# Kernel optimization log

Measured on AMD Instinct MI355X. Metric: run time of the kernel, lower is better.

## Reference

```python
import jax, jax.numpy as jnp
import numpy as np

B, S, HID = 1, 2048, 2048
NH, NKV, HD = 32, 8, 64
ROPE_THETA = 10000.0
NEG = -1e9


def _rope_tables(seq_len, head_dim, theta):
    inv_freq = 1.0 / (theta ** (jnp.arange(0, head_dim, 2, dtype=jnp.float32) / head_dim))
    t = jnp.arange(seq_len, dtype=jnp.float32)
    freqs = jnp.outer(t, inv_freq)            # [S, HD/2]
    emb = jnp.concatenate([freqs, freqs], -1) # [S, HD]
    return jnp.cos(emb), jnp.sin(emb)


def setup_inputs() -> dict:
    key = jax.random.key(0)
    ks = jax.random.split(key, 5)
    sc = 0.02
    hidden_states = jax.random.normal(ks[0], (B, S, HID), jnp.float32)
    Wq = jax.random.normal(ks[1], (NH * HD, HID), jnp.float32) * sc
    Wk = jax.random.normal(ks[2], (NKV * HD, HID), jnp.float32) * sc
    Wv = jax.random.normal(ks[3], (NKV * HD, HID), jnp.float32) * sc
    Wo = jax.random.normal(ks[4], (HID, HID), jnp.float32) * sc
    cos, sin = _rope_tables(S, HD, ROPE_THETA)
    cos = jnp.broadcast_to(cos[None], (B, S, HD))
    sin = jnp.broadcast_to(sin[None], (B, S, HD))
    causal = jnp.tril(jnp.ones((S, S), bool))
    attention_mask = jnp.where(causal, 0.0, NEG).astype(jnp.float32)[None, None]  # [B,1,S,S]
    return {"hidden_states": hidden_states, "Wq": Wq, "Wk": Wk, "Wv": Wv,
            "Wo": Wo, "cos": cos, "sin": sin, "attention_mask": attention_mask}


def _rotate_half(x):
    x1, x2 = jnp.split(x, 2, axis=-1)
    return jnp.concatenate([-x2, x1], axis=-1)


def reference(hidden_states, Wq, Wk, Wv, Wo, cos, sin, attention_mask):
    b, s, _ = hidden_states.shape
    # QKV projections (nn.Linear: x @ W.T), split heads -> [B, H, S, D]
    q = jnp.einsum('bsh,dh->bsd', hidden_states, Wq).reshape(b, s, NH, HD).transpose(0, 2, 1, 3)
    k = jnp.einsum('bsh,dh->bsd', hidden_states, Wk).reshape(b, s, NKV, HD).transpose(0, 2, 1, 3)
    v = jnp.einsum('bsh,dh->bsd', hidden_states, Wv).reshape(b, s, NKV, HD).transpose(0, 2, 1, 3)
    # RoPE (cos/sin broadcast over head dim, unsqueeze_dim=1)
    c = cos[:, None, :, :]
    si = sin[:, None, :, :]
    q = q * c + _rotate_half(q) * si
    k = k * c + _rotate_half(k) * si
    # repeat_kv: GQA groups of 4
    n_rep = NH // NKV
    k = jnp.repeat(k, n_rep, axis=1)
    v = jnp.repeat(v, n_rep, axis=1)
    # Naive materialized attention, softmax in fp32
    scores = jnp.einsum('bhqd,bhkd->bhqk', q, k) / jnp.sqrt(jnp.float32(HD))
    scores = scores + attention_mask
    w = jax.nn.softmax(scores.astype(jnp.float32), axis=-1).astype(q.dtype)
    attn = jnp.einsum('bhqk,bhkd->bhqd', w, v)
    attn = attn.transpose(0, 2, 1, 3).reshape(b, s, NH * HD)
    return jnp.einsum('bsd,od->bso', attn, Wo)
```

## Files before the change

kernel.cpp:

```cpp
#include <hip/hip_runtime.h>
#include <hip/hip_bf16.h>

typedef unsigned short u16;
typedef __bf16 bf16x8 __attribute__((ext_vector_type(8)));
typedef float f32x4 __attribute__((ext_vector_type(4)));

#define S_LEN 2048
#define HID 2048
#define NH 32
#define NKV 8
#define HD 64

__device__ inline u16 f2bf(float x) {
    __bf16 h = (__bf16)x;
    return __builtin_bit_cast(u16, h);
}

__device__ inline void gload_lds16(const u16* g, u16* l) {
    __builtin_amdgcn_global_load_lds((const __attribute__((address_space(1))) unsigned int*)g,
                                     (__attribute__((address_space(3))) unsigned int*)l, 16, 0, 0);
}

__global__ void cvt_all(const float* __restrict__ h, const float* __restrict__ wq,
                        const float* __restrict__ wk, const float* __restrict__ wv,
                        const float* __restrict__ wo,
                        u16* __restrict__ hb, u16* __restrict__ wqkv, u16* __restrict__ wob) {
    int i = blockIdx.x * blockDim.x + threadIdx.x;
    const float* src; u16* dst; int o;
    if (i < 1048576)      { src = h;  dst = hb;   o = i; }
    else if (i < 2097152) { src = wq; dst = wqkv; o = i - 1048576; }
    else if (i < 2359296) { src = wk; dst = wqkv + (size_t)2048 * 2048; o = i - 2097152; }
    else if (i < 2621440) { src = wv; dst = wqkv + (size_t)2560 * 2048; o = i - 2359296; }
    else                  { src = wo; dst = wob;  o = i - 2621440; }
    float4 v = ((const float4*)src)[o];
    ushort4 u;
    u.x = f2bf(v.x); u.y = f2bf(v.y); u.z = f2bf(v.z); u.w = f2bf(v.w);
    ((ushort4*)dst)[o] = u;
}

__global__ __launch_bounds__(256) void gemm_bt(const u16* __restrict__ A,
                                               const u16* __restrict__ B,
                                               void* __restrict__ Cv,
                                               int K_, int mode, int ldc,
                                               const float* __restrict__ cosp,
                                               const float* __restrict__ sinp) {
    __shared__ u16 As[2][64 * 32];
    __shared__ u16 Bs[2][128 * 32];
    const int t = threadIdx.x;
    const int nwg = gridDim.x * gridDim.y;
    const int orig = blockIdx.y * gridDim.x + blockIdx.x;
    const int wgid = (orig & 7) * (nwg >> 3) + (orig >> 3);
    const int bm = wgid % gridDim.x, bn = wgid / gridDim.x;
    const int lane = t & 63, w = t >> 6;
    const int wr2 = (w >> 1) * 32, wc2 = (w & 1) * 64;
    const int g = lane >> 4, r16 = lane & 15;
    f32x4 acc[2][4] = {};

    const int srowA = w * 16 + (lane >> 2);
    const int srowB = w * 32 + (lane >> 2);
    const int scol = (lane & 3) * 8;
    const u16* Ap = A + (size_t)(bm * 64 + srowA) * K_ + scol;
    const u16* Bp = B + (size_t)(bn * 128 + srowB) * K_ + scol;
    const int aoff = w * 512;
    const int boff = w * 1024;

    gload_lds16(Ap, &As[0][aoff]);
    gload_lds16(Bp, &Bs[0][boff]);
    gload_lds16(Bp + (size_t)16 * K_, &Bs[0][boff + 512]);
    __syncthreads();

    int cur = 0;
    for (int kt = 0; kt < K_; kt += 32) {
        const int nxt = kt + 32;
        if (nxt < K_) {
            gload_lds16(Ap + nxt, &As[cur ^ 1][aoff]);
            gload_lds16(Bp + nxt, &Bs[cur ^ 1][boff]);
            gload_lds16(Bp + nxt + (size_t)16 * K_, &Bs[cur ^ 1][boff + 512]);
        }
        bf16x8 af[2], bfr[4];
#pragma unroll
        for (int i = 0; i < 2; i++) af[i] = *(const bf16x8*)(&As[cur][(wr2 + i * 16 + r16) * 32 + g * 8]);
#pragma unroll
        for (int j = 0; j < 4; j++) bfr[j] = *(const bf16x8*)(&Bs[cur][(wc2 + j * 16 + r16) * 32 + g * 8]);
#pragma unroll
        for (int i = 0; i < 2; i++)
#pragma unroll
            for (int j = 0; j < 4; j++)
                acc[i][j] = __builtin_amdgcn_mfma_f32_16x16x32_bf16(af[i], bfr[j], acc[i][j], 0, 0, 0);
        __syncthreads();
        cur ^= 1;
    }

    u16* qb_ = (u16*)Cv;
    u16* kb_ = qb_ + (size_t)2048 * 2048;
    u16* vt_ = kb_ + (size_t)512 * 2048;
    if (mode == 1) {
#pragma unroll
        for (int i = 0; i < 2; i++)
#pragma unroll
            for (int j = 0; j < 4; j++)
#pragma unroll
                for (int r = 0; r < 4; r++) {
                    int row = bm * 64 + wr2 + i * 16 + g * 4 + r;
                    int col = bn * 128 + wc2 + j * 16 + r16;
                    ((float*)Cv)[(size_t)row * ldc + col] = acc[i][j][r];
                }
    } else {
        const int cbase = bn * 128 + wc2;
        if (cbase < 2560) {
            const float scl = (cbase < 2048) ? 0.125f * 1.44269504f : 1.0f;
#pragma unroll
            for (int i = 0; i < 2; i++)
#pragma unroll
                for (int r = 0; r < 4; r++) {
                    int row = bm * 64 + wr2 + i * 16 + g * 4 + r;
#pragma unroll
                    for (int j = 0; j < 2; j++) {
                        int c0 = cbase + j * 16 + r16;
                        int iin = c0 & 63;
                        float x1 = acc[i][j][r], x2 = acc[i][j + 2][r];
                        float cA = cosp[row * 64 + iin],      sA = sinp[row * 64 + iin];
                        float cB = cosp[row * 64 + iin + 32], sB = sinp[row * 64 + iin + 32];
                        u16 o1 = f2bf((x1 * cA - x2 * sA) * scl);
                        u16 o2 = f2bf((x2 * cB + x1 * sB) * scl);
                        if (cbase < 2048) {
                            qb_[(size_t)row * 2048 + c0] = o1;
                            qb_[(size_t)row * 2048 + c0 + 32] = o2;
                        } else {
                            int c = c0 - 2048;
                            int kvh_w = c >> 6, iin2 = c & 63;
                            int gq = (iin2 >> 3) & 3, e = iin2 & 7;
                            int fr = row >> 4, r16w = row & 15;
                            size_t base = ((size_t)(kvh_w * 128 + fr) * 2) * 512 + (size_t)(gq * 16 + r16w) * 8 + e;
                            kb_[base] = o1;
                            kb_[base + 512] = o2;
                        }
                    }
                }
        } else {
#pragma unroll
            for (int i = 0; i < 2; i++)
#pragma unroll
                for (int j = 0; j < 4; j++)
#pragma unroll
                    for (int r = 0; r < 4; r++) {
                        int row = bm * 64 + wr2 + i * 16 + g * 4 + r;
                        int col = cbase + j * 16 + r16;
                        int dg = col - 2560;
                        int kvh_w = dg >> 6, dblk_w = (dg >> 4) & 3, r16v = dg & 15;
                        int fr32 = row >> 5, gv = (row >> 3) & 3, e = row & 7;
                        vt_[((size_t)((kvh_w * 64 + fr32) * 4 + dblk_w)) * 512 + (size_t)(gv * 16 + r16v) * 8 + e] = f2bf(acc[i][j][r]);
                    }
        }
    }
}

__global__ __launch_bounds__(64) void attn_kernel(const u16* __restrict__ q,
                                                  const u16* __restrict__ kp_all,
                                                  const u16* __restrict__ vp_all,
                                                  u16* __restrict__ attn) {
    __shared__ u16 P[2][16][136];
    const int bid = blockIdx.x;
    const int kvh = bid & 7;
    const int h = kvh * 4 + ((bid >> 3) & 3);
    const int p = bid >> 5;
    const int lane = threadIdx.x & 63;
    const int g = lane >> 4, r16 = lane & 15;

    const u16* kp = kp_all + (size_t)kvh * 131072;
    const u16* vp = vp_all + (size_t)kvh * 131072;

    bf16x8 vone;
#pragma unroll
    for (int j = 0; j < 8; j++) vone[j] = (__bf16)1.0f;

    for (int u = 0; u < 2; u++) {
        const int qblk = u ? p : 63 - p;
        const int qrow0 = qblk * 32;

        bf16x8 qf[2][2];
#pragma unroll
        for (int fi = 0; fi < 2; fi++)
#pragma unroll
            for (int d = 0; d < 2; d++)
                qf[fi][d] = *(const bf16x8*)(q + (size_t)(qrow0 + fi * 16 + r16) * (NH * HD) + h * HD + d * 32 + g * 8);

        f32x4 o[2][4] = {};
        f32x4 ol[2] = {};

        const int last = (qrow0 >> 7) << 7;

        bf16x8 kA[4][2], kB[4][2];
#pragma unroll
        for (int s4 = 0; s4 < 4; s4++)
#pragma unroll
            for (int d = 0; d < 2; d++) {
                kA[s4][d] = *(const bf16x8*)(kp + ((size_t)(s4 * 2 + d)) * 512 + lane * 8);
                kB[s4][d] = *(const bf16x8*)(kp + ((size_t)((4 + s4) * 2 + d)) * 512 + lane * 8);
            }

        for (int kv = 0; kv <= last; kv += 128) {
            const bool diag = (kv == last);
            f32x4 sacc[2][8] = {};
#pragma unroll
            for (int s4 = 0; s4 < 4; s4++)
#pragma unroll
                for (int fi = 0; fi < 2; fi++)
#pragma unroll
                    for (int d = 0; d < 2; d++)
                        sacc[fi][s4] = __builtin_amdgcn_mfma_f32_16x16x32_bf16(qf[fi][d], kA[s4][d], sacc[fi][s4], 0, 0, 0);
#pragma unroll
            for (int s4 = 0; s4 < 4; s4++)
#pragma unroll
                for (int fi = 0; fi < 2; fi++)
#pragma unroll
                    for (int d = 0; d < 2; d++)
                        sacc[fi][4 + s4] = __builtin_amdgcn_mfma_f32_16x16x32_bf16(qf[fi][d], kB[s4][d], sacc[fi][4 + s4], 0, 0, 0);
            if (kv + 128 <= last) {
                const int nf = (kv + 128) >> 4;
#pragma unroll
                for (int s4 = 0; s4 < 4; s4++)
#pragma unroll
                    for (int d = 0; d < 2; d++) {
                        kA[s4][d] = *(const bf16x8*)(kp + ((size_t)((nf + s4) * 2 + d)) * 512 + lane * 8);
                        kB[s4][d] = *(const bf16x8*)(kp + ((size_t)((nf + 4 + s4) * 2 + d)) * 512 + lane * 8);
                    }
            }
            bf16x8 vf[4][4];
            const int fv0 = kv >> 5;
#pragma unroll
            for (int kq = 0; kq < 4; kq++)
#pragma unroll
                for (int dblk = 0; dblk < 4; dblk++)
                    vf[kq][dblk] = *(const bf16x8*)(vp + ((size_t)((fv0 + kq) * 4 + dblk)) * 512 + lane * 8);
            if (diag) {
#pragma unroll
                for (int fi = 0; fi < 2; fi++)
#pragma unroll
                    for (int sub = 0; sub < 8; sub++)
#pragma unroll
                        for (int r = 0; r < 4; r++) {
                            int col = kv + sub * 16 + r16;
                            int row = qrow0 + fi * 16 + g * 4 + r;
                            if (col > row) sacc[fi][sub][r] = -1e30f;
                        }
            }
#pragma unroll
            for (int fi = 0; fi < 2; fi++)
#pragma unroll
                for (int sub = 0; sub < 8; sub++)
#pragma unroll
                    for (int r = 0; r < 4; r++)
                        P[fi][g * 4 + r][sub * 16 + r16] = f2bf(__builtin_amdgcn_exp2f(sacc[fi][sub][r]));
#pragma unroll
            for (int fi = 0; fi < 2; fi++)
#pragma unroll
                for (int kq = 0; kq < 4; kq++) {
                    bf16x8 pf = *(const bf16x8*)(&P[fi][r16][kq * 32 + g * 8]);
                    ol[fi] = __builtin_amdgcn_mfma_f32_16x16x32_bf16(pf, vone, ol[fi], 0, 0, 0);
#pragma unroll
                    for (int dblk = 0; dblk < 4; dblk++)
                        o[fi][dblk] = __builtin_amdgcn_mfma_f32_16x16x32_bf16(pf, vf[kq][dblk], o[fi][dblk], 0, 0, 0);
                }
        }
#pragma unroll
        for (int fi = 0; fi < 2; fi++) {
            float inv[4];
#pragma unroll
            for (int r = 0; r < 4; r++) inv[r] = 1.0f / ol[fi][r];
#pragma unroll
            for (int dblk = 0; dblk < 4; dblk++)
#pragma unroll
                for (int r = 0; r < 4; r++) {
                    float val = o[fi][dblk][r] * inv[r];
                    attn[(size_t)(qrow0 + fi * 16 + g * 4 + r) * (NH * HD) + h * HD + dblk * 16 + r16] = f2bf(val);
                }
        }
    }
}

extern "C" void kernel_launch(void* const* d_in, const int* in_sizes, int n_in,
                              void* d_out, int out_size, void* d_ws, size_t ws_size,
                              hipStream_t stream) {
    const float* hidden = (const float*)d_in[0];
    const float* Wq = (const float*)d_in[1];
    const float* Wk = (const float*)d_in[2];
    const float* Wv = (const float*)d_in[3];
    const float* Wo = (const float*)d_in[4];
    const float* cosp = (const float*)d_in[5];
    const float* sinp = (const float*)d_in[6];
    float* out = (float*)d_out;

    char* ws = (char*)d_ws;
    u16* hb   = (u16*)(ws);
    u16* wqkv = (u16*)(ws + ((size_t)8 << 20));
    u16* wob  = (u16*)(ws + ((size_t)20 << 20));
    u16* qbuf = (u16*)(ws + ((size_t)28 << 20));
    u16* kpak = qbuf + (size_t)2048 * 2048;
    u16* vpak = kpak + (size_t)512 * 2048;
    u16* attn = (u16*)(ws + ((size_t)40 << 20));

    cvt_all<<<14336, 256, 0, stream>>>(hidden, Wq, Wk, Wv, Wo, hb, wqkv, wob);

    gemm_bt<<<dim3(32, 24), 256, 0, stream>>>(hb, wqkv, qbuf, HID, 3, 0, cosp, sinp);

    attn_kernel<<<S_LEN / 64 * NH, 64, 0, stream>>>(qbuf, kpak, vpak, attn);

    gemm_bt<<<dim3(32, 16), 256, 0, stream>>>(attn, wob, out, HID, 1, HID, nullptr, nullptr);

    (void)in_sizes; (void)n_in; (void)out_size; (void)ws_size;
}
```

Measured before the change: 137.5 us.

## Pre-pack GEMM operands into tile-contiguous layout for coalesced LDS loads

```diff
diff --git a/kernel.cpp b/kernel.cpp
--- a/kernel.cpp
+++ b/kernel.cpp
@@ -21,25 +21,31 @@
                                      (__attribute__((address_space(3))) unsigned int*)l, 16, 0, 0);
 }
 
+
 __global__ void cvt_all(const float* __restrict__ h, const float* __restrict__ wq,
                         const float* __restrict__ wk, const float* __restrict__ wv,
                         const float* __restrict__ wo,
                         u16* __restrict__ hb, u16* __restrict__ wqkv, u16* __restrict__ wob) {
     int i = blockIdx.x * blockDim.x + threadIdx.x;
-    const float* src; u16* dst; int o;
+    const float* src; u16* dst; int o; int rowoff = 0;
     if (i < 1048576)      { src = h;  dst = hb;   o = i; }
     else if (i < 2097152) { src = wq; dst = wqkv; o = i - 1048576; }
-    else if (i < 2359296) { src = wk; dst = wqkv + (size_t)2048 * 2048; o = i - 2097152; }
-    else if (i < 2621440) { src = wv; dst = wqkv + (size_t)2560 * 2048; o = i - 2359296; }
+    else if (i < 2359296) { src = wk; dst = wqkv; o = i - 2097152; rowoff = 2048; }
+    else if (i < 2621440) { src = wv; dst = wqkv; o = i - 2359296; rowoff = 2560; }
     else                  { src = wo; dst = wob;  o = i - 2621440; }
     float4 v = ((const float4*)src)[o];
     ushort4 u;
     u.x = f2bf(v.x); u.y = f2bf(v.y); u.z = f2bf(v.z); u.w = f2bf(v.w);
-    ((ushort4*)dst)[o] = u;
-}
-
-__global__ __launch_bounds__(256) void gemm_bt(const u16* __restrict__ A,
-                                               const u16* __restrict__ B,
+    const int row = (o >> 9) + rowoff;
+    const int col0 = (o & 511) * 4;
+    const int fr = row >> 4, r16w = row & 15;
+    const int kc = col0 >> 5, gq = (col0 >> 3) & 3, e = col0 & 7;
+    u16* d = dst + ((size_t)(fr * 64 + kc) * 64 + r16w * 4 + gq) * 8 + e;
+    *(ushort4*)d = u;
+}
+
+__global__ __launch_bounds__(256) void gemm_bt(const u16* __restrict__ Apk,
+                                               const u16* __restrict__ Bpk,
                                                void* __restrict__ Cv,
                                                int K_, int mode, int ldc,
                                                const float* __restrict__ cosp,
@@ -54,28 +60,26 @@
     const int lane = t & 63, w = t >> 6;
     const int wr2 = (w >> 1) * 32, wc2 = (w & 1) * 64;
     const int g = lane >> 4, r16 = lane & 15;
+    const int K32 = K_ >> 5;
     f32x4 acc[2][4] = {};
 
-    const int srowA = w * 16 + (lane >> 2);
-    const int srowB = w * 32 + (lane >> 2);
-    const int scol = (lane & 3) * 8;
-    const u16* Ap = A + (size_t)(bm * 64 + srowA) * K_ + scol;
-    const u16* Bp = B + (size_t)(bn * 128 + srowB) * K_ + scol;
+    const u16* Ap = Apk + ((size_t)(bm * 4 + w) * K32) * 512 + lane * 8;
+    const u16* Bp0 = Bpk + ((size_t)(bn * 8 + w * 2) * K32) * 512 + lane * 8;
+    const u16* Bp1 = Bpk + ((size_t)(bn * 8 + w * 2 + 1) * K32) * 512 + lane * 8;
     const int aoff = w * 512;
     const int boff = w * 1024;
 
     gload_lds16(Ap, &As[0][aoff]);
-    gload_lds16(Bp, &Bs[0][boff]);
-    gload_lds16(Bp + (size_t)16 * K_, &Bs[0][boff + 512]);
+    gload_lds16(Bp0, &Bs[0][boff]);
+    gload_lds16(Bp1, &Bs[0][boff + 512]);
     __syncthreads();
 
     int cur = 0;
-    for (int kt = 0; kt < K_; kt += 32) {
-        const int nxt = kt + 32;
-        if (nxt < K_) {
-            gload_lds16(Ap + nxt, &As[cur ^ 1][aoff]);
-            gload_lds16(Bp + nxt, &Bs[cur ^ 1][boff]);
-            gload_lds16(Bp + nxt + (size_t)16 * K_, &Bs[cur ^ 1][boff + 512]);
+    for (int kc = 0; kc < K32; kc++) {
+        if (kc + 1 < K32) {
+            gload_lds16(Ap + (size_t)(kc + 1) * 512, &As[cur ^ 1][aoff]);
+            gload_lds16(Bp0 + (size_t)(kc + 1) * 512, &Bs[cur ^ 1][boff]);
+            gload_lds16(Bp1 + (size_t)(kc + 1) * 512, &Bs[cur ^ 1][boff + 512]);
         }
         bf16x8 af[2], bfr[4];
 #pragma unroll
@@ -158,7 +162,7 @@
 __global__ __launch_bounds__(64) void attn_kernel(const u16* __restrict__ q,
                                                   const u16* __restrict__ kp_all,
                                                   const u16* __restrict__ vp_all,
-                                                  u16* __restrict__ attn) {
+                                                  u16* __restrict__ attn_pk) {
     __shared__ u16 P[2][16][136];
     const int bid = blockIdx.x;
     const int kvh = bid & 7;
@@ -268,13 +272,18 @@
             float inv[4];
 #pragma unroll
             for (int r = 0; r < 4; r++) inv[r] = 1.0f / ol[fi][r];
-#pragma unroll
-            for (int dblk = 0; dblk < 4; dblk++)
+            const int fr = qblk * 2 + fi;
+#pragma unroll
+            for (int dblk = 0; dblk < 4; dblk++) {
+                const int kc = h * 2 + (dblk >> 1);
+                const int ls_base = (dblk & 1) * 2 + (r16 >> 3);
+                const int e = r16 & 7;
 #pragma unroll
                 for (int r = 0; r < 4; r++) {
                     float val = o[fi][dblk][r] * inv[r];
-                    attn[(size_t)(qrow0 + fi * 16 + g * 4 + r) * (NH * HD) + h * HD + dblk * 16 + r16] = f2bf(val);
+                    attn_pk[((size_t)(fr * 64 + kc) * 64 + (g * 4 + r) * 4 + ls_base) * 8 + e] = f2bf(val);
                 }
+            }
         }
     }
 }
@@ -298,15 +307,15 @@
     u16* qbuf = (u16*)(ws + ((size_t)28 << 20));
     u16* kpak = qbuf + (size_t)2048 * 2048;
     u16* vpak = kpak + (size_t)512 * 2048;
-    u16* attn = (u16*)(ws + ((size_t)40 << 20));
+    u16* atpk = (u16*)(ws + ((size_t)40 << 20));
 
     cvt_all<<<14336, 256, 0, stream>>>(hidden, Wq, Wk, Wv, Wo, hb, wqkv, wob);
 
     gemm_bt<<<dim3(32, 24), 256, 0, stream>>>(hb, wqkv, qbuf, HID, 3, 0, cosp, sinp);
 
-    attn_kernel<<<S_LEN / 64 * NH, 64, 0, stream>>>(qbuf, kpak, vpak, attn);
-
-    gemm_bt<<<dim3(32, 16), 256, 0, stream>>>(attn, wob, out, HID, 1, HID, nullptr, nullptr);
+    attn_kernel<<<S_LEN / 64 * NH, 64, 0, stream>>>(qbuf, kpak, vpak, atpk);
+
+    gemm_bt<<<dim3(32, 16), 256, 0, stream>>>(atpk, wob, out, HID, 1, HID, nullptr, nullptr);
 
     (void)in_sizes; (void)n_in; (void)out_size; (void)ws_size;
 }
```

New measurement: 136.4 us. Within noise of the previous version (-0.8%).
